# Kernel optimization log

Hardware: AMD Instinct MI355X
Metric: run time of the kernel (lower is better)

Reference implementation:

```python
import jax, jax.numpy as jnp
import numpy as np

T, N, DEG = 8, 8192, 15
H = 4


def _gat(x, src, dst, wl, wr, a, b):
    """GATv2Conv with concat=False (heads averaged). x: [N, Cin] -> [N, Cout].
    e_ij = a_h . LeakyReLU(Wl x_j + Wr x_i); softmax over incoming edges of i;
    messages are Wl x_j (PyG GATv2 convention, self-loops already in edge list)."""
    n = x.shape[0]
    h, c = a.shape
    gl = (x @ wl).reshape(n, h, c)  # source-side transform
    gr = (x @ wr).reshape(n, h, c)  # target-side transform
    z = jax.nn.leaky_relu(gl[src] + gr[dst], 0.2)          # [E,H,C]
    e = jnp.einsum('ehc,hc->eh', z, a)                     # [E,H]
    m = jax.ops.segment_max(e, dst, num_segments=n)        # [N,H]
    ex = jnp.exp(e - m[dst])
    den = jax.ops.segment_sum(ex, dst, num_segments=n)     # [N,H]
    msg = jax.ops.segment_sum(ex[:, :, None] * gl[src], dst, num_segments=n)
    return (msg / den[:, :, None]).mean(axis=1) + b


def _d3(x, esrc, edst, wl, wr, a, b):
    # spatio-temporal graph conv: GATv2 applied independently per timestep
    return jax.lax.map(lambda args: _gat(args[0], args[1], args[2], wl, wr, a, b),
                       (x, esrc, edst))


def setup_inputs() -> dict:
    key = jax.random.key(0)
    ks = iter(jax.random.split(key, 32))
    x = jax.random.normal(next(ks), (T, N, 64), dtype=jnp.float32)
    # fixed-degree random graph per timestep + self loops (PyG add_self_loops=True)
    dst_base = jnp.repeat(jnp.arange(N, dtype=jnp.int32), DEG)
    src_r = jax.random.randint(next(ks), (T, N * DEG), 0, N, dtype=jnp.int32)
    loop = jnp.arange(N, dtype=jnp.int32)
    edge_src = jnp.concatenate([src_r, jnp.broadcast_to(loop, (T, N))], axis=1)
    edge_dst = jnp.concatenate([jnp.broadcast_to(dst_base, (T, N * DEG)),
                                jnp.broadcast_to(loop, (T, N))], axis=1)

    def gat_p(k, cin, cout):
        k1, k2, k3 = jax.random.split(k, 3)
        s = 1.0 / np.sqrt(cin)
        return ((jax.random.normal(k1, (cin, H * cout)) * s).astype(jnp.float32),
                (jax.random.normal(k2, (cin, H * cout)) * s).astype(jnp.float32),
                (jax.random.normal(k3, (H, cout)) * s).astype(jnp.float32),
                jnp.zeros((cout,), jnp.float32))

    inp = {"x": x, "edge_src": edge_src, "edge_dst": edge_dst}
    for name, cin, cout in [("c1", 64, 128), ("c2", 128, 64), ("c3", 64, 64), ("c4", 128, 64),
                            ("r11", 64, 64), ("r12", 64, 64), ("r2", 128, 128),
                            ("f11", 64, 64), ("f2", 128, 128)]:
        wl, wr, a, b = gat_p(next(ks), cin, cout)
        inp[name + "_wl"], inp[name + "_wr"], inp[name + "_a"], inp[name + "_b"] = wl, wr, a, b
    # ConvTranspose1d(k=1) == per-node linear conv_ch -> in_channels; then Linear in_channels -> original_dim
    for name, cin, cout in [("r3", 128, 64), ("f3", 128, 64), ("r4", 64, 64), ("f4", 64, 64)]:
        inp[name + "_w"] = (jax.random.normal(next(ks), (cin, cout)) * (1.0 / np.sqrt(cin))).astype(jnp.float32)
        inp[name + "_b"] = jnp.zeros((cout,), jnp.float32)
    return inp


def reference(x, edge_src, edge_dst,
              c1_wl, c1_wr, c1_a, c1_b, c2_wl, c2_wr, c2_a, c2_b,
              c3_wl, c3_wr, c3_a, c3_b, c4_wl, c4_wr, c4_a, c4_b,
              r11_wl, r11_wr, r11_a, r11_b, r12_wl, r12_wr, r12_a, r12_b,
              r2_wl, r2_wr, r2_a, r2_b, r3_w, r3_b, r4_w, r4_b,
              f11_wl, f11_wr, f11_a, f11_b, f2_wl, f2_wr, f2_a, f2_b,
              f3_w, f3_b, f4_w, f4_b):
    elu = jax.nn.elu
    out = elu(_d3(x, edge_src, edge_dst, c1_wl, c1_wr, c1_a, c1_b))           # [T,N,128]
    emb = elu(_d3(out, edge_src, edge_dst, c2_wl, c2_wr, c2_a, c2_b))         # [T,N,64]
    emb = elu(jnp.concatenate([_d3(emb, edge_src, edge_dst, c3_wl, c3_wr, c3_a, c3_b), emb], -1))  # [T,N,128]
    emb = elu(_d3(emb, edge_src, edge_dst, c4_wl, c4_wr, c4_a, c4_b))         # [T,N,64]

    # reconstruction branch on edges at t = -1
    s1, d1 = edge_src[-1], edge_dst[-1]
    r = elu(_gat(emb[-1], s1, d1, r11_wl, r11_wr, r11_a, r11_b))
    r = elu(jnp.concatenate([_gat(r, s1, d1, r12_wl, r12_wr, r12_a, r12_b), r], -1))  # [N,128]
    # F.dropout in eval mode -> identity
    r = elu(_gat(r, s1, d1, r2_wl, r2_wr, r2_a, r2_b))
    r = jnp.tanh(r @ r3_w + r3_b)
    recon = r @ r4_w + r4_b

    # forecasting branch on edges at t = -2 (original reuses reconstruct12 here)
    s2, d2 = edge_src[-2], edge_dst[-2]
    f = elu(_gat(emb[-2], s2, d2, f11_wl, f11_wr, f11_a, f11_b))
    f = elu(jnp.concatenate([_gat(f, s2, d2, r12_wl, r12_wr, r12_a, r12_b), f], -1))
    f = elu(_gat(f, s2, d2, f2_wl, f2_wr, f2_a, f2_b))
    f = jnp.tanh(f @ f3_w + f3_b)
    forecast = f @ f4_w + f4_b
    return (recon, forecast, emb)
```

## Files before the change

### kernel.cpp

```cpp
#include <hip/hip_runtime.h>
#include <cmath>

constexpr int T_   = 8;
constexpr int N_   = 8192;
constexpr int DEG_ = 15;
constexpr int E_   = N_ * (DEG_ + 1);
constexpr float L2E_ = 1.44269504f;

__device__ __forceinline__ float elu1(float v) { return v > 0.f ? v : expm1f(v); }

typedef __attribute__((ext_vector_type(8))) short bf16x8;
typedef __attribute__((ext_vector_type(4))) float f32x4;

__device__ __forceinline__ ushort f2bf(float x) {
  uint u = __float_as_uint(x);
  return (ushort)((u + 0x7FFFu + ((u >> 16) & 1u)) >> 16);
}
__device__ __forceinline__ float bf2f(ushort h) {
  return __uint_as_float(((uint)h) << 16);
}

__global__ __launch_bounds__(256) void split_x(
    const float* __restrict__ X, ushort* __restrict__ XH, ushort* __restrict__ XL, int n4)
{
  const int i = blockIdx.x * 256 + threadIdx.x;
  if (i >= n4) return;
  const float4 v = ((const float4*)X)[i];
  const ushort h0 = f2bf(v.x), h1 = f2bf(v.y), h2 = f2bf(v.z), h3 = f2bf(v.w);
  ushort4 hh; hh.x = h0; hh.y = h1; hh.z = h2; hh.w = h3;
  ushort4 ll;
  ll.x = f2bf(v.x - bf2f(h0)); ll.y = f2bf(v.y - bf2f(h1));
  ll.z = f2bf(v.z - bf2f(h2)); ll.w = f2bf(v.w - bf2f(h3));
  ((ushort4*)XH)[i] = hh;
  ((ushort4*)XL)[i] = ll;
}

__global__ __launch_bounds__(256) void split_wt(
    const float* __restrict__ Wl, const float* __restrict__ Wr,
    ushort* __restrict__ WH, ushort* __restrict__ WL, int K, int HC)
{
  const int idx = blockIdx.x * 256 + threadIdx.x;
  if (idx >= 2 * HC * K) return;
  const int k = idx % K;
  const int n = (idx / K) % HC;
  const int s = idx / (K * HC);
  const float v = (s ? Wr : Wl)[k * HC + n];
  const ushort h = f2bf(v);
  WH[idx] = h;
  WL[idx] = f2bf(v - bf2f(h));
}

__global__ __launch_bounds__(256) void gemm_mfma(
    const ushort* __restrict__ Ah, const ushort* __restrict__ Al,
    const ushort* __restrict__ Wh, const ushort* __restrict__ Wl,
    float* __restrict__ Cl, float* __restrict__ Cr,
    int M, int Ncol, int K, int nt)
{
  __shared__ alignas(16) ushort lAh[4 * 1032];
  __shared__ alignas(16) ushort lAl[4 * 1032];
  __shared__ alignas(16) ushort lBh[4 * 520];
  __shared__ alignas(16) ushort lBl[4 * 520];

  const int z = blockIdx.z;
  const int t = (z < nt) ? z : z - nt;
  const int side = (z < nt) ? 0 : 1;
  const ushort* __restrict__ Bh = Wh + (size_t)side * Ncol * K;
  const ushort* __restrict__ Bl = Wl + (size_t)side * Ncol * K;
  float* __restrict__ C = (side ? Cr : Cl) + (size_t)t * M * Ncol;
  const size_t aoff = (size_t)t * M * K;

  const int bm = blockIdx.x * 128, bn = blockIdx.y * 64;
  const int tid = threadIdx.x;
  const int wid = tid >> 6, lane = tid & 63;
  const int l15 = lane & 15, lk = lane >> 4;

  f32x4 acc[2][4] = {};

  for (int k0 = 0; k0 < K; k0 += 32) {
    #pragma unroll
    for (int c = 0; c < 2; c++) {
      const int ch = tid + c * 256;
      const int row = ch >> 2, kc = ch & 3;
      const size_t ga = aoff + (size_t)(bm + row) * K + (k0 + kc * 8);
      *(uint4*)&lAh[kc * 1032 + row * 8] = *(const uint4*)(Ah + ga);
      *(uint4*)&lAl[kc * 1032 + row * 8] = *(const uint4*)(Al + ga);
    }
    {
      const int col = tid >> 2, kc = tid & 3;
      const size_t gb = (size_t)(bn + col) * K + (k0 + kc * 8);
      *(uint4*)&lBh[kc * 520 + col * 8] = *(const uint4*)(Bh + gb);
      *(uint4*)&lBl[kc * 520 + col * 8] = *(const uint4*)(Bl + gb);
    }
    __syncthreads();

    bf16x8 ah[2], al[2], bh4[4], bl4[4];
    const int r0 = wid * 32;
    #pragma unroll
    for (int rf = 0; rf < 2; rf++) {
      const int ro = (r0 + rf * 16 + l15) * 8;
      ah[rf] = *(const bf16x8*)&lAh[lk * 1032 + ro];
      al[rf] = *(const bf16x8*)&lAl[lk * 1032 + ro];
    }
    #pragma unroll
    for (int cf = 0; cf < 4; cf++) {
      const int co = (cf * 16 + l15) * 8;
      bh4[cf] = *(const bf16x8*)&lBh[lk * 520 + co];
      bl4[cf] = *(const bf16x8*)&lBl[lk * 520 + co];
    }
    #pragma unroll
    for (int rf = 0; rf < 2; rf++)
      #pragma unroll
      for (int cf = 0; cf < 4; cf++) {
        acc[rf][cf] = __builtin_amdgcn_mfma_f32_16x16x32_bf16(ah[rf], bh4[cf], acc[rf][cf], 0, 0, 0);
        acc[rf][cf] = __builtin_amdgcn_mfma_f32_16x16x32_bf16(ah[rf], bl4[cf], acc[rf][cf], 0, 0, 0);
        acc[rf][cf] = __builtin_amdgcn_mfma_f32_16x16x32_bf16(al[rf], bh4[cf], acc[rf][cf], 0, 0, 0);
      }
    __syncthreads();
  }

  #pragma unroll
  for (int rf = 0; rf < 2; rf++)
    #pragma unroll
    for (int cf = 0; cf < 4; cf++) {
      const int col = bn + cf * 16 + l15;
      #pragma unroll
      for (int reg = 0; reg < 4; reg++) {
        const int row = bm + wid * 32 + rf * 16 + lk * 4 + reg;
        C[(size_t)row * Ncol + col] = acc[rf][cf][reg];
      }
    }
}

template<int EPI>
__global__ __launch_bounds__(256) void gemm_k(
    const float* __restrict__ A, const float* __restrict__ B,
    float* __restrict__ C, const float* __restrict__ bias,
    int M, int Ncol, int K)
{
  __shared__ float As[16][68];
  __shared__ float Bs[16][64];

  const int tid = threadIdx.x;
  const int tx = tid & 15, ty = tid >> 4;
  const int bm = blockIdx.x * 64, bn = blockIdx.y * 64;

  const int arow = tid >> 2;
  const int akc  = (tid & 3) * 4;
  const int brow = tid >> 4;
  const int bc4  = (tid & 15) * 4;

  float acc[4][4];
  #pragma unroll
  for (int i = 0; i < 4; i++)
    #pragma unroll
    for (int j = 0; j < 4; j++) acc[i][j] = 0.f;

  for (int k0 = 0; k0 < K; k0 += 16) {
    const float4 va = *(const float4*)(A + (size_t)(bm + arow) * K + (k0 + akc));
    const float4 vb = *(const float4*)(B + (size_t)(k0 + brow) * Ncol + (bn + bc4));
    As[akc + 0][arow] = va.x; As[akc + 1][arow] = va.y;
    As[akc + 2][arow] = va.z; As[akc + 3][arow] = va.w;
    *(float4*)&Bs[brow][bc4] = vb;
    __syncthreads();
    #pragma unroll
    for (int kk = 0; kk < 16; kk++) {
      const float4 av = *(const float4*)&As[kk][ty * 4];
      const float4 bv = *(const float4*)&Bs[kk][tx * 4];
      const float a4[4] = {av.x, av.y, av.z, av.w};
      const float b4[4] = {bv.x, bv.y, bv.z, bv.w};
      #pragma unroll
      for (int i = 0; i < 4; i++)
        #pragma unroll
        for (int j = 0; j < 4; j++)
          acc[i][j] = fmaf(a4[i], b4[j], acc[i][j]);
    }
    __syncthreads();
  }

  #pragma unroll
  for (int i = 0; i < 4; i++) {
    const int row = bm + ty * 4 + i;
    const int col = bn + tx * 4;
    float v[4] = {acc[i][0], acc[i][1], acc[i][2], acc[i][3]};
    #pragma unroll
    for (int j = 0; j < 4; j++) v[j] += bias[col + j];
    if (EPI == 1) {
      #pragma unroll
      for (int j = 0; j < 4; j++) v[j] = tanhf(v[j]);
    }
    *(float4*)(C + (size_t)row * Ncol + col) = make_float4(v[0], v[1], v[2], v[3]);
  }
}

template<bool CONCAT>
__global__ __launch_bounds__(256) void gat_agg256(
    const float* __restrict__ GL, const float* __restrict__ GR,
    const float* __restrict__ aw_, const float* __restrict__ bias,
    const int* __restrict__ esrc, float* __restrict__ out,
    const float* __restrict__ csrc, int numNodes)
{
  constexpr int HC = 256, C = 64;
  constexpr int OSTR = CONCAT ? 128 : 64;

  const int lane = threadIdx.x & 63;
  const int wid  = threadIdx.x >> 6;
  const int gid  = blockIdx.x * 4 + wid;
  if (gid >= numNodes) return;
  const int t = gid >> 13;
  const int i = gid & (N_ - 1);

  const float* __restrict__ gl = GL + (size_t)t * N_ * HC;
  const int*   __restrict__ es = esrc + (size_t)t * E_ + (size_t)i * DEG_;

  float gr[4], a6[4], a4c[4];
  {
    const float4 gv = *(const float4*)(GR + (size_t)gid * HC + lane * 4);
    const float4 av = *(const float4*)(aw_ + lane * 4);
    gr[0] = gv.x; gr[1] = gv.y; gr[2] = gv.z; gr[3] = gv.w;
    a6[0] = 0.6f * av.x; a6[1] = 0.6f * av.y; a6[2] = 0.6f * av.z; a6[3] = 0.6f * av.w;
    a4c[0] = 0.4f * av.x; a4c[1] = 0.4f * av.y; a4c[2] = 0.4f * av.z; a4c[3] = 0.4f * av.w;
  }

  float acc[4] = {0.f, 0.f, 0.f, 0.f};
  float den = 0.f, m = -1e30f;

  #pragma unroll
  for (int b = 0; b < 4; b++) {
    int js[4];
    #pragma unroll
    for (int q = 0; q < 4; q++) {
      const int ek = b * 4 + q;
      js[q] = (ek < DEG_) ? es[ek] : i;
    }
    float g[4][4];
    #pragma unroll
    for (int q = 0; q < 4; q++) {
      const float4 v = *(const float4*)(gl + (size_t)js[q] * HC + lane * 4);
      g[q][0] = v.x; g[q][1] = v.y; g[q][2] = v.z; g[q][3] = v.w;
    }
    float p[4];
    #pragma unroll
    for (int q = 0; q < 4; q++) {
      float s = 0.f;
      #pragma unroll
      for (int u = 0; u < 4; u++) {
        const float z = g[q][u] + gr[u];
        s = fmaf(z, a6[u], s);
        s = fmaf(fabsf(z), a4c[u], s);
      }
      p[q] = s;
    }
    #pragma unroll
    for (int q = 0; q < 4; q++) {
      p[q] += __shfl_xor(p[q], 1);
      p[q] += __shfl_xor(p[q], 2);
      p[q] += __shfl_xor(p[q], 4);
      p[q] += __shfl_xor(p[q], 8);
    }
    const float bmax = fmaxf(fmaxf(p[0], p[1]), fmaxf(p[2], p[3]));
    const float nm   = fmaxf(m, bmax);
    const float sc   = exp2f((m - nm) * L2E_);
    den *= sc;
    #pragma unroll
    for (int u = 0; u < 4; u++) acc[u] *= sc;
    #pragma unroll
    for (int q = 0; q < 4; q++) {
      const float w = exp2f((p[q] - nm) * L2E_);
      den += w;
      #pragma unroll
      for (int u = 0; u < 4; u++) acc[u] = fmaf(w, g[q][u], acc[u]);
    }
    m = nm;
  }

  const float inv = 1.f / den;
  #pragma unroll
  for (int u = 0; u < 4; u++) acc[u] *= inv;
  #pragma unroll
  for (int u = 0; u < 4; u++) {
    acc[u] += __shfl_xor(acc[u], 16);
    acc[u] += __shfl_xor(acc[u], 32);
  }

  float* orow = out + (size_t)gid * OSTR;
  if (lane < 16) {
    #pragma unroll
    for (int u = 0; u < 4; u++)
      acc[u] = elu1(acc[u] * 0.25f + bias[lane * 4 + u]);
    *(float4*)(orow + lane * 4) = make_float4(acc[0], acc[1], acc[2], acc[3]);
  } else if (CONCAT && lane < 32) {
    const int q = lane - 16;
    const float4 v = *(const float4*)(csrc + (size_t)gid * C + q * 4);
    *(float4*)(orow + C + q * 4) =
        make_float4(elu1(v.x), elu1(v.y), elu1(v.z), elu1(v.w));
  }
}

__global__ __launch_bounds__(256) void gat_agg512(
    const float* __restrict__ GL, const float* __restrict__ GR,
    const float* __restrict__ aw_, const float* __restrict__ bias,
    const int* __restrict__ esrc, float* __restrict__ out)
{
  __shared__ float smem[4][128];

  const int lane = threadIdx.x & 63;
  const int h    = threadIdx.x >> 6;
  const int gid  = blockIdx.x;
  const int t = gid >> 13;
  const int i = gid & (N_ - 1);

  const float* __restrict__ gl = GL + (size_t)t * N_ * 512;
  const int*   __restrict__ es = esrc + (size_t)t * E_ + (size_t)i * DEG_;
  const int cb = h * 128 + lane * 2;

  float gr0, gr1, a60, a61, a40, a41;
  {
    const float2 gv = *(const float2*)(GR + (size_t)gid * 512 + cb);
    const float2 av = *(const float2*)(aw_ + cb);
    gr0 = gv.x; gr1 = gv.y;
    a60 = 0.6f * av.x; a61 = 0.6f * av.y;
    a40 = 0.4f * av.x; a41 = 0.4f * av.y;
  }

  float acc0 = 0.f, acc1 = 0.f, den = 0.f, m = -1e30f;

  #pragma unroll
  for (int b = 0; b < 4; b++) {
    int js[4];
    #pragma unroll
    for (int q = 0; q < 4; q++) {
      const int ek = b * 4 + q;
      js[q] = (ek < DEG_) ? es[ek] : i;
    }
    float g[4][2];
    #pragma unroll
    for (int q = 0; q < 4; q++) {
      const float2 v = *(const float2*)(gl + (size_t)js[q] * 512 + cb);
      g[q][0] = v.x; g[q][1] = v.y;
    }
    float p[4];
    #pragma unroll
    for (int q = 0; q < 4; q++) {
      const float z0 = g[q][0] + gr0;
      const float z1 = g[q][1] + gr1;
      float s = z0 * a60;
      s = fmaf(fabsf(z0), a40, s);
      s = fmaf(z1, a61, s);
      s = fmaf(fabsf(z1), a41, s);
      p[q] = s;
    }
    #pragma unroll
    for (int q = 0; q < 4; q++) {
      p[q] += __shfl_xor(p[q], 1);
      p[q] += __shfl_xor(p[q], 2);
      p[q] += __shfl_xor(p[q], 4);
      p[q] += __shfl_xor(p[q], 8);
      p[q] += __shfl_xor(p[q], 16);
      p[q] += __shfl_xor(p[q], 32);
    }
    const float bmax = fmaxf(fmaxf(p[0], p[1]), fmaxf(p[2], p[3]));
    const float nm   = fmaxf(m, bmax);
    const float sc   = exp2f((m - nm) * L2E_);
    den *= sc; acc0 *= sc; acc1 *= sc;
    #pragma unroll
    for (int q = 0; q < 4; q++) {
      const float w = exp2f((p[q] - nm) * L2E_);
      den += w;
      acc0 = fmaf(w, g[q][0], acc0);
      acc1 = fmaf(w, g[q][1], acc1);
    }
    m = nm;
  }

  const float inv = 1.f / den;
  smem[h][lane * 2]     = acc0 * inv;
  smem[h][lane * 2 + 1] = acc1 * inv;
  __syncthreads();

  if (h == 0) {
    const int c = lane * 2;
    float s0 = smem[0][c] + smem[1][c] + smem[2][c] + smem[3][c];
    float s1 = smem[0][c + 1] + smem[1][c + 1] + smem[2][c + 1] + smem[3][c + 1];
    s0 = elu1(s0 * 0.25f + bias[c]);
    s1 = elu1(s1 * 0.25f + bias[c + 1]);
    *(float2*)(out + (size_t)gid * 128 + c) = make_float2(s0, s1);
  }
}

extern "C" void kernel_launch(void* const* d_in, const int* in_sizes, int n_in,
                              void* d_out, int out_size, void* d_ws, size_t ws_size,
                              hipStream_t stream)
{
  (void)in_sizes; (void)n_in; (void)out_size; (void)ws_size;

  const float* x  = (const float*)d_in[0];
  const int*   es = (const int*)d_in[1];
  const float *c1_wl=(const float*)d_in[3], *c1_wr=(const float*)d_in[4], *c1_a=(const float*)d_in[5], *c1_b=(const float*)d_in[6];
  const float *c2_wl=(const float*)d_in[7], *c2_wr=(const float*)d_in[8], *c2_a=(const float*)d_in[9], *c2_b=(const float*)d_in[10];
  const float *c3_wl=(const float*)d_in[11],*c3_wr=(const float*)d_in[12],*c3_a=(const float*)d_in[13],*c3_b=(const float*)d_in[14];
  const float *c4_wl=(const float*)d_in[15],*c4_wr=(const float*)d_in[16],*c4_a=(const float*)d_in[17],*c4_b=(const float*)d_in[18];
  const float *r11_wl=(const float*)d_in[19],*r11_wr=(const float*)d_in[20],*r11_a=(const float*)d_in[21],*r11_b=(const float*)d_in[22];
  const float *r12_wl=(const float*)d_in[23],*r12_wr=(const float*)d_in[24],*r12_a=(const float*)d_in[25],*r12_b=(const float*)d_in[26];
  const float *r2_wl=(const float*)d_in[27],*r2_wr=(const float*)d_in[28],*r2_a=(const float*)d_in[29],*r2_b=(const float*)d_in[30];
  const float *f11_wl=(const float*)d_in[31],*f11_wr=(const float*)d_in[32],*f11_a=(const float*)d_in[33],*f11_b=(const float*)d_in[34];
  const float *f2_wl=(const float*)d_in[35],*f2_wr=(const float*)d_in[36],*f2_a=(const float*)d_in[37],*f2_b=(const float*)d_in[38];
  const float *r3_w=(const float*)d_in[39], *r3_b=(const float*)d_in[40];
  const float *f3_w=(const float*)d_in[41], *f3_b=(const float*)d_in[42];
  const float *r4_w=(const float*)d_in[43], *r4_b=(const float*)d_in[44];
  const float *f4_w=(const float*)d_in[45], *f4_b=(const float*)d_in[46];

  float* ws = (float*)d_ws;
  float* GL = ws;
  float* GR = GL + (size_t)16777216;
  float* A0 = GR + (size_t)16777216;
  float* A1 = A0 + (size_t)T_ * N_ * 128;
  float* B0 = A1 + (size_t)T_ * N_ * 64;
  float* B1 = B0 + (size_t)N_ * 128;
  ushort* SH = (ushort*)(B1 + (size_t)N_ * 128);
  ushort* SL = SH + (size_t)8388608;
  ushort* WH = SL + (size_t)8388608;
  ushort* WL = WH + (size_t)131072;

  float* recon = (float*)d_out;
  float* fcst  = recon + (size_t)N_ * 64;
  float* emb   = fcst + (size_t)N_ * 64;

  const dim3 blk(256);

  split_x<<<dim3((T_ * N_ * 64 / 4 + 255) / 256), blk, 0, stream>>>(x, SH, SL, T_ * N_ * 64 / 4);
  split_wt<<<dim3((2 * 512 * 64 + 255) / 256), blk, 0, stream>>>(c1_wl, c1_wr, WH, WL, 64, 512);
  for (int ch = 0; ch < 2; ch++) {
    const int t0 = ch * 4, nt = 4;
    gemm_mfma<<<dim3(N_ / 128, 8, 2 * nt), blk, 0, stream>>>(
        SH + (size_t)t0 * N_ * 64, SL + (size_t)t0 * N_ * 64, WH, WL, GL, GR, N_, 512, 64, nt);
    gat_agg512<<<dim3(nt * N_), blk, 0, stream>>>(
        GL, GR, c1_a, c1_b, es + (size_t)t0 * E_, A0 + (size_t)t0 * N_ * 128);
  }
  split_x<<<dim3((T_ * N_ * 128 / 4 + 255) / 256), blk, 0, stream>>>(A0, SH, SL, T_ * N_ * 128 / 4);
  split_wt<<<dim3((2 * 256 * 128 + 255) / 256), blk, 0, stream>>>(c2_wl, c2_wr, WH, WL, 128, 256);
  gemm_mfma<<<dim3(N_ / 128, 4, 2 * T_), blk, 0, stream>>>(SH, SL, WH, WL, GL, GR, N_, 256, 128, T_);
  gat_agg256<false><<<dim3(T_ * N_ / 4), blk, 0, stream>>>(GL, GR, c2_a, c2_b, es, A1, nullptr, T_ * N_);
  split_x<<<dim3((T_ * N_ * 64 / 4 + 255) / 256), blk, 0, stream>>>(A1, SH, SL, T_ * N_ * 64 / 4);
  split_wt<<<dim3((2 * 256 * 64 + 255) / 256), blk, 0, stream>>>(c3_wl, c3_wr, WH, WL, 64, 256);
  gemm_mfma<<<dim3(N_ / 128, 4, 2 * T_), blk, 0, stream>>>(SH, SL, WH, WL, GL, GR, N_, 256, 64, T_);
  gat_agg256<true><<<dim3(T_ * N_ / 4), blk, 0, stream>>>(GL, GR, c3_a, c3_b, es, A0, A1, T_ * N_);
  split_x<<<dim3((T_ * N_ * 128 / 4 + 255) / 256), blk, 0, stream>>>(A0, SH, SL, T_ * N_ * 128 / 4);
  split_wt<<<dim3((2 * 256 * 128 + 255) / 256), blk, 0, stream>>>(c4_wl, c4_wr, WH, WL, 128, 256);
  gemm_mfma<<<dim3(N_ / 128, 4, 2 * T_), blk, 0, stream>>>(SH, SL, WH, WL, GL, GR, N_, 256, 128, T_);
  gat_agg256<false><<<dim3(T_ * N_ / 4), blk, 0, stream>>>(GL, GR, c4_a, c4_b, es, emb, nullptr, T_ * N_);

  const float* embR = emb + (size_t)7 * N_ * 64;
  const int*   esR  = es + (size_t)7 * E_;
  split_x<<<dim3((N_ * 64 / 4 + 255) / 256), blk, 0, stream>>>(embR, SH, SL, N_ * 64 / 4);
  split_wt<<<dim3((2 * 256 * 64 + 255) / 256), blk, 0, stream>>>(r11_wl, r11_wr, WH, WL, 64, 256);
  gemm_mfma<<<dim3(N_ / 128, 4, 2), blk, 0, stream>>>(SH, SL, WH, WL, GL, GR, N_, 256, 64, 1);
  gat_agg256<false><<<dim3(N_ / 4), blk, 0, stream>>>(GL, GR, r11_a, r11_b, esR, B0, nullptr, N_);
  split_x<<<dim3((N_ * 64 / 4 + 255) / 256), blk, 0, stream>>>(B0, SH, SL, N_ * 64 / 4);
  split_wt<<<dim3((2 * 256 * 64 + 255) / 256), blk, 0, stream>>>(r12_wl, r12_wr, WH, WL, 64, 256);
  gemm_mfma<<<dim3(N_ / 128, 4, 2), blk, 0, stream>>>(SH, SL, WH, WL, GL, GR, N_, 256, 64, 1);
  gat_agg256<true><<<dim3(N_ / 4), blk, 0, stream>>>(GL, GR, r12_a, r12_b, esR, B1, B0, N_);
  split_x<<<dim3((N_ * 128 / 4 + 255) / 256), blk, 0, stream>>>(B1, SH, SL, N_ * 128 / 4);
  split_wt<<<dim3((2 * 512 * 128 + 255) / 256), blk, 0, stream>>>(r2_wl, r2_wr, WH, WL, 128, 512);
  gemm_mfma<<<dim3(N_ / 128, 8, 2), blk, 0, stream>>>(SH, SL, WH, WL, GL, GR, N_, 512, 128, 1);
  gat_agg512<<<dim3(N_), blk, 0, stream>>>(GL, GR, r2_a, r2_b, esR, B0);
  gemm_k<1><<<dim3(N_ / 64, 1, 1), blk, 0, stream>>>(B0, r3_w, B1, r3_b, N_, 64, 128);
  gemm_k<2><<<dim3(N_ / 64, 1, 1), blk, 0, stream>>>(B1, r4_w, recon, r4_b, N_, 64, 64);

  const float* embF = emb + (size_t)6 * N_ * 64;
  const int*   esF  = es + (size_t)6 * E_;
  split_x<<<dim3((N_ * 64 / 4 + 255) / 256), blk, 0, stream>>>(embF, SH, SL, N_ * 64 / 4);
  split_wt<<<dim3((2 * 256 * 64 + 255) / 256), blk, 0, stream>>>(f11_wl, f11_wr, WH, WL, 64, 256);
  gemm_mfma<<<dim3(N_ / 128, 4, 2), blk, 0, stream>>>(SH, SL, WH, WL, GL, GR, N_, 256, 64, 1);
  gat_agg256<false><<<dim3(N_ / 4), blk, 0, stream>>>(GL, GR, f11_a, f11_b, esF, B0, nullptr, N_);
  split_x<<<dim3((N_ * 64 / 4 + 255) / 256), blk, 0, stream>>>(B0, SH, SL, N_ * 64 / 4);
  split_wt<<<dim3((2 * 256 * 64 + 255) / 256), blk, 0, stream>>>(r12_wl, r12_wr, WH, WL, 64, 256);
  gemm_mfma<<<dim3(N_ / 128, 4, 2), blk, 0, stream>>>(SH, SL, WH, WL, GL, GR, N_, 256, 64, 1);
  gat_agg256<true><<<dim3(N_ / 4), blk, 0, stream>>>(GL, GR, r12_a, r12_b, esF, B1, B0, N_);
  split_x<<<dim3((N_ * 128 / 4 + 255) / 256), blk, 0, stream>>>(B1, SH, SL, N_ * 128 / 4);
  split_wt<<<dim3((2 * 512 * 128 + 255) / 256), blk, 0, stream>>>(f2_wl, f2_wr, WH, WL, 128, 512);
  gemm_mfma<<<dim3(N_ / 128, 8, 2), blk, 0, stream>>>(SH, SL, WH, WL, GL, GR, N_, 512, 128, 1);
  gat_agg512<<<dim3(N_), blk, 0, stream>>>(GL, GR, f2_a, f2_b, esF, B0);
  gemm_k<1><<<dim3(N_ / 64, 1, 1), blk, 0, stream>>>(B0, f3_w, B1, f3_b, N_, 64, 128);
  gemm_k<2><<<dim3(N_ / 64, 1, 1), blk, 0, stream>>>(B1, f4_w, fcst, f4_b, N_, 64, 64);
}
```

Baseline: 1.073 ms.

## Split gat_agg512 wavefront into four edge groups with wider per-lane channel vectors

The 512-wide aggregation kernel now has each wavefront split into four 16-lane groups. Each group handles four of the sixteen incoming edges, and each lane covers 8 channels through float4 loads instead of 2 channels through float2 loads. The online-softmax sequential loop is replaced by a single global max across groups, followed by a second pass that re-gathers the neighbor rows for the weighted sum and ends in cross-group shuffle reductions. This cuts the serial dependency chain and shuffle count per edge and widens the memory accesses. In exchange, every gathered row is read twice from memory or cache and register use per lane goes up.

```diff
diff --git a/kernel.cpp b/kernel.cpp
--- a/kernel.cpp
+++ b/kernel.cpp
@@ -311,70 +311,107 @@
 
   const float* __restrict__ gl = GL + (size_t)t * N_ * 512;
   const int*   __restrict__ es = esrc + (size_t)t * E_ + (size_t)i * DEG_;
-  const int cb = h * 128 + lane * 2;
-
-  float gr0, gr1, a60, a61, a40, a41;
+
+  const int grp = lane >> 4;
+  const int s   = lane & 15;
+  const int cb  = h * 128 + s * 8;
+
+  float gr[8], a6[8], a4[8];
   {
-    const float2 gv = *(const float2*)(GR + (size_t)gid * 512 + cb);
-    const float2 av = *(const float2*)(aw_ + cb);
-    gr0 = gv.x; gr1 = gv.y;
-    a60 = 0.6f * av.x; a61 = 0.6f * av.y;
-    a40 = 0.4f * av.x; a41 = 0.4f * av.y;
-  }
-
-  float acc0 = 0.f, acc1 = 0.f, den = 0.f, m = -1e30f;
-
-  #pragma unroll
-  for (int b = 0; b < 4; b++) {
-    int js[4];
-    #pragma unroll
-    for (int q = 0; q < 4; q++) {
-      const int ek = b * 4 + q;
-      js[q] = (ek < DEG_) ? es[ek] : i;
-    }
-    float g[4][2];
-    #pragma unroll
-    for (int q = 0; q < 4; q++) {
-      const float2 v = *(const float2*)(gl + (size_t)js[q] * 512 + cb);
-      g[q][0] = v.x; g[q][1] = v.y;
-    }
-    float p[4];
-    #pragma unroll
-    for (int q = 0; q < 4; q++) {
-      const float z0 = g[q][0] + gr0;
-      const float z1 = g[q][1] + gr1;
-      float s = z0 * a60;
-      s = fmaf(fabsf(z0), a40, s);
-      s = fmaf(z1, a61, s);
-      s = fmaf(fabsf(z1), a41, s);
-      p[q] = s;
-    }
-    #pragma unroll
-    for (int q = 0; q < 4; q++) {
-      p[q] += __shfl_xor(p[q], 1);
-      p[q] += __shfl_xor(p[q], 2);
-      p[q] += __shfl_xor(p[q], 4);
-      p[q] += __shfl_xor(p[q], 8);
-      p[q] += __shfl_xor(p[q], 16);
-      p[q] += __shfl_xor(p[q], 32);
-    }
-    const float bmax = fmaxf(fmaxf(p[0], p[1]), fmaxf(p[2], p[3]));
-    const float nm   = fmaxf(m, bmax);
-    const float sc   = exp2f((m - nm) * L2E_);
-    den *= sc; acc0 *= sc; acc1 *= sc;
-    #pragma unroll
-    for (int q = 0; q < 4; q++) {
-      const float w = exp2f((p[q] - nm) * L2E_);
-      den += w;
-      acc0 = fmaf(w, g[q][0], acc0);
-      acc1 = fmaf(w, g[q][1], acc1);
-    }
-    m = nm;
+    const float4 g0 = *(const float4*)(GR + (size_t)gid * 512 + cb);
+    const float4 g1 = *(const float4*)(GR + (size_t)gid * 512 + cb + 4);
+    gr[0] = g0.x; gr[1] = g0.y; gr[2] = g0.z; gr[3] = g0.w;
+    gr[4] = g1.x; gr[5] = g1.y; gr[6] = g1.z; gr[7] = g1.w;
+    const float4 a0 = *(const float4*)(aw_ + cb);
+    const float4 a1 = *(const float4*)(aw_ + cb + 4);
+    a6[0] = 0.6f * a0.x; a6[1] = 0.6f * a0.y; a6[2] = 0.6f * a0.z; a6[3] = 0.6f * a0.w;
+    a6[4] = 0.6f * a1.x; a6[5] = 0.6f * a1.y; a6[6] = 0.6f * a1.z; a6[7] = 0.6f * a1.w;
+    a4[0] = 0.4f * a0.x; a4[1] = 0.4f * a0.y; a4[2] = 0.4f * a0.z; a4[3] = 0.4f * a0.w;
+    a4[4] = 0.4f * a1.x; a4[5] = 0.4f * a1.y; a4[6] = 0.4f * a1.z; a4[7] = 0.4f * a1.w;
+  }
+
+  int js[4];
+  #pragma unroll
+  for (int q = 0; q < 4; q++) {
+    const int ek = grp * 4 + q;
+    js[q] = (ek < DEG_) ? es[ek] : i;
+  }
+
+  float p[4];
+  #pragma unroll
+  for (int b = 0; b < 2; b++) {
+    float gq[2][8];
+    #pragma unroll
+    for (int q = 0; q < 2; q++) {
+      const float* gp = gl + (size_t)js[b * 2 + q] * 512 + cb;
+      const float4 v0 = *(const float4*)gp;
+      const float4 v1 = *(const float4*)(gp + 4);
+      gq[q][0] = v0.x; gq[q][1] = v0.y; gq[q][2] = v0.z; gq[q][3] = v0.w;
+      gq[q][4] = v1.x; gq[q][5] = v1.y; gq[q][6] = v1.z; gq[q][7] = v1.w;
+    }
+    #pragma unroll
+    for (int q = 0; q < 2; q++) {
+      float sc = 0.f;
+      #pragma unroll
+      for (int u = 0; u < 8; u++) {
+        const float z = gq[q][u] + gr[u];
+        sc = fmaf(z, a6[u], sc);
+        sc = fmaf(fabsf(z), a4[u], sc);
+      }
+      p[b * 2 + q] = sc;
+    }
+  }
+  #pragma unroll
+  for (int q = 0; q < 4; q++) {
+    p[q] += __shfl_xor(p[q], 1);
+    p[q] += __shfl_xor(p[q], 2);
+    p[q] += __shfl_xor(p[q], 4);
+    p[q] += __shfl_xor(p[q], 8);
+  }
+  float M = fmaxf(fmaxf(p[0], p[1]), fmaxf(p[2], p[3]));
+  M = fmaxf(M, __shfl_xor(M, 16));
+  M = fmaxf(M, __shfl_xor(M, 32));
+
+  float w[4];
+  float den = 0.f;
+  #pragma unroll
+  for (int q = 0; q < 4; q++) { w[q] = exp2f((p[q] - M) * L2E_); den += w[q]; }
+
+  float acc[8] = {0.f, 0.f, 0.f, 0.f, 0.f, 0.f, 0.f, 0.f};
+  #pragma unroll
+  for (int b = 0; b < 2; b++) {
+    float gq[2][8];
+    #pragma unroll
+    for (int q = 0; q < 2; q++) {
+      const float* gp = gl + (size_t)js[b * 2 + q] * 512 + cb;
+      const float4 v0 = *(const float4*)gp;
+      const float4 v1 = *(const float4*)(gp + 4);
+      gq[q][0] = v0.x; gq[q][1] = v0.y; gq[q][2] = v0.z; gq[q][3] = v0.w;
+      gq[q][4] = v1.x; gq[q][5] = v1.y; gq[q][6] = v1.z; gq[q][7] = v1.w;
+    }
+    #pragma unroll
+    for (int q = 0; q < 2; q++)
+      #pragma unroll
+      for (int u = 0; u < 8; u++)
+        acc[u] = fmaf(w[b * 2 + q], gq[q][u], acc[u]);
+  }
+
+  den += __shfl_xor(den, 16);
+  den += __shfl_xor(den, 32);
+  #pragma unroll
+  for (int u = 0; u < 8; u++) {
+    acc[u] += __shfl_xor(acc[u], 16);
+    acc[u] += __shfl_xor(acc[u], 32);
   }
 
   const float inv = 1.f / den;
-  smem[h][lane * 2]     = acc0 * inv;
-  smem[h][lane * 2 + 1] = acc1 * inv;
+  if (grp == 0) {
+    float o[8];
+    #pragma unroll
+    for (int u = 0; u < 8; u++) o[u] = acc[u] * inv;
+    *(float4*)&smem[h][s * 8]     = make_float4(o[0], o[1], o[2], o[3]);
+    *(float4*)&smem[h][s * 8 + 4] = make_float4(o[4], o[5], o[6], o[7]);
+  }
   __syncthreads();
 
   if (h == 0) {
```

After: 1.408 ms. +31.2%, slower.
